# Optimization experiments

Hardware: AMD Instinct MI355X
Metric: run time of the kernel (lower is better)

## Reference

```python
import jax, jax.numpy as jnp
import numpy as np

B, L, D_MODEL = 2, 2048, 1024
EXPAND, D_STATE, D_CONV = 2, 16, 4
D_INNER = EXPAND * D_MODEL
DT_RANK = D_MODEL // 16  # mamba default: ceil(d_model/16)


def setup_inputs() -> dict:
    key = jax.random.key(0)
    ks = jax.random.split(key, 8)
    s = 0.02
    return {
        "x": jax.random.normal(ks[0], (B, L, D_MODEL), jnp.float32),
        "in_proj_w": jax.random.normal(ks[1], (2 * D_INNER, D_MODEL), jnp.float32) * s,
        "conv_w": jax.random.normal(ks[2], (D_INNER, D_CONV), jnp.float32) * s,
        "conv_b": jnp.zeros((D_INNER,), jnp.float32),
        "x_proj_w": jax.random.normal(ks[3], (DT_RANK + 2 * D_STATE, D_INNER), jnp.float32) * s,
        "dt_proj_w": jax.random.normal(ks[4], (D_INNER, DT_RANK), jnp.float32) * s,
        "dt_proj_b": jnp.full((D_INNER,), -4.6, jnp.float32),  # softplus(-4.6) ~ 0.01 dt init
        "A_log": jnp.log(jnp.broadcast_to(jnp.arange(1, D_STATE + 1, dtype=jnp.float32), (D_INNER, D_STATE))),
        "D": jnp.ones((D_INNER,), jnp.float32),
        "ssm_out_w": jax.random.normal(ks[5], (D_MODEL, D_INNER), jnp.float32) * s,
        "final_w": jax.random.normal(ks[6], (D_MODEL, D_MODEL), jnp.float32) * s,
        "final_b": jnp.zeros((D_MODEL,), jnp.float32),
    }


def _forward(x, in_proj_w, conv_w, conv_b, x_proj_w, dt_proj_w, dt_proj_b,
             A_log, D, ssm_out_w, final_w, final_b):
    d_inner, d_state = A_log.shape
    dt_rank = dt_proj_w.shape[1]
    d_conv = conv_w.shape[1]

    # in_proj -> split into x-branch and gate z  (B, L, 2*d_inner)
    xz = jnp.einsum('bld,ed->ble', x, in_proj_w)
    xin, z = jnp.split(xz, 2, axis=-1)

    # causal depthwise conv1d over time, then SiLU
    xc = jax.lax.conv_general_dilated(
        xin.swapaxes(1, 2),               # (B, d_inner, L)
        conv_w[:, None, :],               # (O=d_inner, I/g=1, W=d_conv)
        window_strides=(1,),
        padding=[(d_conv - 1, 0)],
        dimension_numbers=('NCH', 'OIH', 'NCH'),
        feature_group_count=d_inner,
    )
    xc = jax.nn.silu(xc + conv_b[None, :, None]).swapaxes(1, 2)  # (B, L, d_inner)

    # input-dependent SSM parameters
    x_dbl = jnp.einsum('bld,ed->ble', xc, x_proj_w)              # (B, L, dt_rank+2*d_state)
    dt, Bm, Cm = jnp.split(x_dbl, [dt_rank, dt_rank + d_state], axis=-1)
    delta = jax.nn.softplus(jnp.einsum('blr,dr->bld', dt, dt_proj_w) + dt_proj_b)  # (B,L,d_inner)
    A = -jnp.exp(A_log)                                          # (d_inner, d_state)

    # selective scan: h_t = exp(dt*A) h_{t-1} + dt*B_t*u_t ; y_t = <h_t, C_t>
    def step(h, t):
        delta_t, B_t, C_t, u_t = t                               # (B,Di), (B,N), (B,N), (B,Di)
        h = jnp.exp(delta_t[..., None] * A) * h + (delta_t * u_t)[..., None] * B_t[:, None, :]
        return h, jnp.einsum('bdn,bn->bd', h, C_t)

    h0 = jnp.zeros((x.shape[0], d_inner, d_state), x.dtype)
    xs = (delta.swapaxes(0, 1), Bm.swapaxes(0, 1), Cm.swapaxes(0, 1), xc.swapaxes(0, 1))
    _, ys = jax.lax.scan(step, h0, xs)                           # (L, B, d_inner)

    y = ys.swapaxes(0, 1) + xc * D                               # skip term D*u
    y = y * jax.nn.silu(z)                                       # gating
    out = jnp.einsum('bld,md->blm', y, ssm_out_w)                # Mamba out_proj -> d_model
    # wrapper: Linear(d_model, d_model) then SiLU
    return jax.nn.silu(jnp.einsum('blm,nm->bln', out, final_w) + final_b)


def reference(x, in_proj_w, conv_w, conv_b, x_proj_w, dt_proj_w, dt_proj_b,
              A_log, D, ssm_out_w, final_w, final_b):
    return _forward(x, in_proj_w, conv_w, conv_b, x_proj_w, dt_proj_w, dt_proj_b,
                    A_log, D, ssm_out_w, final_w, final_b)
```

## Files before the change

kernel.cpp:

```cpp
#include <hip/hip_runtime.h>
#include <hip/hip_bf16.h>
#include <math.h>

#define BB 2
#define LL 2048
#define DMODEL 1024
#define DINNER 2048
#define DSTATE 16
#define DCONV 4
#define DTRANK 64
#define MROWS (BB * LL)
#define XPROJ_N (DTRANK + 2 * DSTATE)

#define SEG 64
#define LS (LL / SEG)

#define XKSPLIT 8
#define XKC (DINNER / XKSPLIT)

typedef unsigned short ushort_t;
typedef short s8v __attribute__((ext_vector_type(8)));
typedef float f4v __attribute__((ext_vector_type(4)));

__device__ __forceinline__ float siluf(float x) {
    return x / (1.f + expf(-x));
}
__device__ __forceinline__ float softplusf(float x) {
    return fmaxf(x, 0.f) + log1pf(expf(-fabsf(x)));
}
__device__ __forceinline__ ushort_t f32_to_bf16(float f) {
    unsigned u = __builtin_bit_cast(unsigned, f);
    unsigned r = (u + 0x7FFFu + ((u >> 16) & 1u)) >> 16;
    return (ushort_t)r;
}
__device__ __forceinline__ float bf16_to_f32(ushort_t u) {
    return __builtin_bit_cast(float, ((unsigned)u) << 16);
}

__global__ __launch_bounds__(256) void prep_kernel(
    const float* __restrict__ x, const float* __restrict__ ipw,
    const float* __restrict__ sow, const float* __restrict__ fw,
    const float* __restrict__ xpw, const float* __restrict__ dtw,
    ushort_t* __restrict__ x_bf, ushort_t* __restrict__ ipw_bf,
    ushort_t* __restrict__ sow_bf, ushort_t* __restrict__ fw_bf,
    ushort_t* __restrict__ xpw_bf, ushort_t* __restrict__ dtw_bf,
    float4* __restrict__ xdbl_zero)
{
    const long i = ((long)blockIdx.x * 256 + threadIdx.x) * 4;
    const float* src; ushort_t* dst; long off;
    if      (i < 4194304L)  { src = x;   dst = x_bf;   off = i; }
    else if (i < 8388608L)  { src = ipw; dst = ipw_bf; off = i - 4194304L; }
    else if (i < 10485760L) { src = sow; dst = sow_bf; off = i - 8388608L; }
    else if (i < 11534336L) { src = fw;  dst = fw_bf;  off = i - 10485760L; }
    else if (i < 11730944L) { src = xpw; dst = xpw_bf; off = i - 11534336L; }
    else if (i < 11862016L) { src = dtw; dst = dtw_bf; off = i - 11730944L; }
    else { xdbl_zero[(i - 11862016L) >> 2] = make_float4(0.f, 0.f, 0.f, 0.f); return; }
    const float4 v = *reinterpret_cast<const float4*>(src + off);
    ushort_t o[4] = {f32_to_bf16(v.x), f32_to_bf16(v.y),
                     f32_to_bf16(v.z), f32_to_bf16(v.w)};
    *reinterpret_cast<uint2*>(dst + off) = *reinterpret_cast<uint2*>(o);
}

__global__ __launch_bounds__(256) void cast_dt_kernel(
    const float* __restrict__ xdbl, ushort_t* __restrict__ dtbf)
{
    const int i4 = (blockIdx.x * 256 + threadIdx.x) * 4;
    const int row = i4 >> 6;
    const int col = i4 & 63;
    const float4 v = *reinterpret_cast<const float4*>(&xdbl[(size_t)row * XPROJ_N + col]);
    ushort_t o[4] = {f32_to_bf16(v.x), f32_to_bf16(v.y),
                     f32_to_bf16(v.z), f32_to_bf16(v.w)};
    *reinterpret_cast<uint2*>(dtbf + i4) = *reinterpret_cast<uint2*>(o);
}

#define TM 128
#define TN 128
#define TBK 32

__global__ __launch_bounds__(512) void gemm_bf16_mfma(
    const ushort_t* __restrict__ A, int lda,
    const ushort_t* __restrict__ B, int ldb,
    int K,
    void* __restrict__ C0v, void* __restrict__ C1v, int splitN, int ldc,
    const float* __restrict__ bias, int act, int store_bf16)
{
    __shared__ __align__(16) ushort_t As[TM * TBK];
    __shared__ __align__(16) ushort_t Bs[TN * TBK];

    const int tid  = threadIdx.x;
    const int lane = tid & 63;
    const int w    = tid >> 6;
    const int wm   = w & 1;
    const int wn   = w >> 1;
    const int m0   = blockIdx.y * TM;
    const int n0   = blockIdx.x * TN;

    const int srow = lane >> 2;
    const int scol = (lane & 3) * 8;

    f4v acc[4][2] = {};

    for (int k0 = 0; k0 < K; k0 += TBK) {
        {
            const ushort_t* ga = A + (size_t)(m0 + w * 16 + srow) * lda + k0 + scol;
            __builtin_amdgcn_global_load_lds(
                (const __attribute__((address_space(1))) unsigned int*)ga,
                (__attribute__((address_space(3))) unsigned int*)(As + w * 512),
                16, 0, 0);
        }
        {
            const ushort_t* gb = B + (size_t)(n0 + w * 16 + srow) * ldb + k0 + scol;
            __builtin_amdgcn_global_load_lds(
                (const __attribute__((address_space(1))) unsigned int*)gb,
                (__attribute__((address_space(3))) unsigned int*)(Bs + w * 512),
                16, 0, 0);
        }
        __syncthreads();

        const int fr = lane & 15;
        const int kg = lane >> 4;
        s8v a[4], b[2];
        #pragma unroll
        for (int t = 0; t < 4; ++t)
            a[t] = *reinterpret_cast<const s8v*>(As + (wm * 64 + t * 16 + fr) * TBK + kg * 8);
        #pragma unroll
        for (int t = 0; t < 2; ++t)
            b[t] = *reinterpret_cast<const s8v*>(Bs + (wn * 32 + t * 16 + fr) * TBK + kg * 8);
        #pragma unroll
        for (int i = 0; i < 4; ++i)
            #pragma unroll
            for (int j = 0; j < 2; ++j)
                acc[i][j] = __builtin_amdgcn_mfma_f32_16x16x32_bf16(
                    a[i], b[j], acc[i][j], 0, 0, 0);
        __syncthreads();
    }

    const int rbase = (lane >> 4) * 4;
    const int cbase = lane & 15;
    #pragma unroll
    for (int i = 0; i < 4; ++i) {
        #pragma unroll
        for (int j = 0; j < 2; ++j) {
            const int row = m0 + wm * 64 + i * 16 + rbase;
            const int col = n0 + wn * 32 + j * 16 + cbase;
            void* Cp = C0v;
            int c2 = col;
            if (C1v && col >= splitN) { Cp = C1v; c2 = col - splitN; }
            const float bv = bias ? bias[col] : 0.f;
            #pragma unroll
            for (int r = 0; r < 4; ++r) {
                float v = acc[i][j][r] + bv;
                if (act == 1) v = siluf(v);
                else if (act == 2) v = softplusf(v);
                if (store_bf16)
                    ((ushort_t*)Cp)[(size_t)(row + r) * ldc + c2] = f32_to_bf16(v);
                else
                    ((float*)Cp)[(size_t)(row + r) * ldc + c2] = v;
            }
        }
    }
}

#define UM 64
#define UN 128

__global__ __launch_bounds__(512) void gemm64_bf16_mfma(
    const ushort_t* __restrict__ A, int lda,
    const ushort_t* __restrict__ B, int ldb,
    int K,
    void* __restrict__ C0v, int ldc,
    const float* __restrict__ bias, int act, int store_bf16)
{
    __shared__ __align__(16) ushort_t As[UM * TBK];
    __shared__ __align__(16) ushort_t Bs[UN * TBK];

    const int tid  = threadIdx.x;
    const int lane = tid & 63;
    const int w    = tid >> 6;
    const int wm   = w & 1;
    const int wn   = w >> 1;
    const int m0   = blockIdx.y * UM;
    const int n0   = blockIdx.x * UN;

    const int srow = lane >> 2;
    const int scol = (lane & 3) * 8;

    f4v acc[2][2] = {};

    for (int k0 = 0; k0 < K; k0 += TBK) {
        if (w < 4) {
            const ushort_t* ga = A + (size_t)(m0 + w * 16 + srow) * lda + k0 + scol;
            __builtin_amdgcn_global_load_lds(
                (const __attribute__((address_space(1))) unsigned int*)ga,
                (__attribute__((address_space(3))) unsigned int*)(As + w * 512),
                16, 0, 0);
        }
        {
            const ushort_t* gb = B + (size_t)(n0 + w * 16 + srow) * ldb + k0 + scol;
            __builtin_amdgcn_global_load_lds(
                (const __attribute__((address_space(1))) unsigned int*)gb,
                (__attribute__((address_space(3))) unsigned int*)(Bs + w * 512),
                16, 0, 0);
        }
        __syncthreads();

        const int fr = lane & 15;
        const int kg = lane >> 4;
        s8v a[2], b[2];
        #pragma unroll
        for (int t = 0; t < 2; ++t)
            a[t] = *reinterpret_cast<const s8v*>(As + (wm * 32 + t * 16 + fr) * TBK + kg * 8);
        #pragma unroll
        for (int t = 0; t < 2; ++t)
            b[t] = *reinterpret_cast<const s8v*>(Bs + (wn * 32 + t * 16 + fr) * TBK + kg * 8);
        #pragma unroll
        for (int i = 0; i < 2; ++i)
            #pragma unroll
            for (int j = 0; j < 2; ++j)
                acc[i][j] = __builtin_amdgcn_mfma_f32_16x16x32_bf16(
                    a[i], b[j], acc[i][j], 0, 0, 0);
        __syncthreads();
    }

    const int rbase = (lane >> 4) * 4;
    const int cbase = lane & 15;
    #pragma unroll
    for (int i = 0; i < 2; ++i) {
        #pragma unroll
        for (int j = 0; j < 2; ++j) {
            const int row = m0 + wm * 32 + i * 16 + rbase;
            const int col = n0 + wn * 32 + j * 16 + cbase;
            const float bv = bias ? bias[col] : 0.f;
            #pragma unroll
            for (int r = 0; r < 4; ++r) {
                float v = acc[i][j][r] + bv;
                if (act == 1) v = siluf(v);
                else if (act == 2) v = softplusf(v);
                if (store_bf16)
                    ((ushort_t*)C0v)[(size_t)(row + r) * ldc + col] = f32_to_bf16(v);
                else
                    ((float*)C0v)[(size_t)(row + r) * ldc + col] = v;
            }
        }
    }
}

__global__ __launch_bounds__(256) void xproj_mfma(
    const ushort_t* __restrict__ A, const ushort_t* __restrict__ Bw,
    float* __restrict__ Cout)
{
    __shared__ __align__(16) ushort_t As[64 * 32];
    __shared__ __align__(16) ushort_t Bs[96 * 32];

    const int tid = threadIdx.x;
    const int lane = tid & 63;
    const int w = tid >> 6;
    const int kbase = blockIdx.x * XKC;
    const int m0 = blockIdx.y * 64;

    const int srow = lane >> 2;
    const int scol = (lane & 3) * 8;

    f4v acc[6] = {};

    for (int k0 = kbase; k0 < kbase + XKC; k0 += 32) {
        {
            const ushort_t* ga = A + (size_t)(m0 + w * 16 + srow) * DINNER + k0 + scol;
            __builtin_amdgcn_global_load_lds(
                (const __attribute__((address_space(1))) unsigned int*)ga,
                (__attribute__((address_space(3))) unsigned int*)(As + (w * 16) * 32),
                16, 0, 0);
        }
        {
            const ushort_t* gb = Bw + (size_t)(w * 16 + srow) * DINNER + k0 + scol;
            __builtin_amdgcn_global_load_lds(
                (const __attribute__((address_space(1))) unsigned int*)gb,
                (__attribute__((address_space(3))) unsigned int*)(Bs + (w * 16) * 32),
                16, 0, 0);
        }
        if (w < 2) {
            const ushort_t* gb = Bw + (size_t)((4 + w) * 16 + srow) * DINNER + k0 + scol;
            __builtin_amdgcn_global_load_lds(
                (const __attribute__((address_space(1))) unsigned int*)gb,
                (__attribute__((address_space(3))) unsigned int*)(Bs + ((4 + w) * 16) * 32),
                16, 0, 0);
        }
        __syncthreads();

        const int fr = lane & 15;
        const int kg = lane >> 4;
        const s8v a = *reinterpret_cast<const s8v*>(As + (w * 16 + fr) * 32 + kg * 8);
        #pragma unroll
        for (int j = 0; j < 6; ++j) {
            const s8v b = *reinterpret_cast<const s8v*>(Bs + (j * 16 + fr) * 32 + kg * 8);
            acc[j] = __builtin_amdgcn_mfma_f32_16x16x32_bf16(a, b, acc[j], 0, 0, 0);
        }
        __syncthreads();
    }

    const int rbase = (lane >> 4) * 4;
    const int cb = lane & 15;
    #pragma unroll
    for (int j = 0; j < 6; ++j)
        #pragma unroll
        for (int r = 0; r < 4; ++r)
            atomicAdd(&Cout[(size_t)(m0 + w * 16 + rbase + r) * XPROJ_N + j * 16 + cb],
                      acc[j][r]);
}

__global__ __launch_bounds__(256) void conv_silu_kernel(
    const ushort_t* __restrict__ xin, const float* __restrict__ w,
    const float* __restrict__ b, ushort_t* __restrict__ xcbf)
{
    const int idx = blockIdx.x * blockDim.x + threadIdx.x;
    const int c = idx % DINNER;
    const int bl = idx / DINNER;
    const int l = bl % LL;
    const int bb = bl / LL;
    if (bb >= BB) return;

    const ushort_t* xp = xin + (size_t)bb * LL * DINNER + c;
    float acc = b[c];
    #pragma unroll
    for (int k = 0; k < DCONV; ++k) {
        const int ll = l - (DCONV - 1) + k;
        if (ll >= 0)
            acc = fmaf(bf16_to_f32(xp[(size_t)ll * DINNER]), w[c * DCONV + k], acc);
    }
    xcbf[idx] = f32_to_bf16(siluf(acc));
}

__global__ __launch_bounds__(256) void scan_part1(
    const ushort_t* __restrict__ delta, const float* __restrict__ xdbl,
    const ushort_t* __restrict__ xc, const float* __restrict__ A_log,
    float* __restrict__ hloc, float* __restrict__ decay)
{
    const int d = blockIdx.x * 256 + threadIdx.x;
    const int seg = blockIdx.y;
    const int b = blockIdx.z;
    const int t0 = seg * LS;

    float Ad[DSTATE];
    #pragma unroll
    for (int n = 0; n < DSTATE; ++n)
        Ad[n] = -expf(A_log[d * DSTATE + n]);

    float h[DSTATE];
    #pragma unroll
    for (int n = 0; n < DSTATE; ++n) h[n] = 0.f;

    const ushort_t* dp = delta + ((size_t)b * LL) * DINNER + d;
    const ushort_t* up = xc    + ((size_t)b * LL) * DINNER + d;
    const float*    xb = xdbl  + ((size_t)b * LL) * XPROJ_N;

    float sum_dl = 0.f;
    for (int t = t0; t < t0 + LS; ++t) {
        const float dl = bf16_to_f32(dp[(size_t)t * DINNER]);
        const float u  = bf16_to_f32(up[(size_t)t * DINNER]);
        const float4 b0 = *reinterpret_cast<const float4*>(&xb[t * XPROJ_N + DTRANK + 0]);
        const float4 b1 = *reinterpret_cast<const float4*>(&xb[t * XPROJ_N + DTRANK + 4]);
        const float4 b2 = *reinterpret_cast<const float4*>(&xb[t * XPROJ_N + DTRANK + 8]);
        const float4 b3 = *reinterpret_cast<const float4*>(&xb[t * XPROJ_N + DTRANK + 12]);
        const float Bv[DSTATE] = {b0.x, b0.y, b0.z, b0.w, b1.x, b1.y, b1.z, b1.w,
                                  b2.x, b2.y, b2.z, b2.w, b3.x, b3.y, b3.z, b3.w};
        const float dlu = dl * u;
        sum_dl += dl;
        #pragma unroll
        for (int n = 0; n < DSTATE; ++n)
            h[n] = __expf(dl * Ad[n]) * h[n] + dlu * Bv[n];
    }

    const size_t base = (((size_t)b * SEG + seg) * DSTATE) * DINNER + d;
    #pragma unroll
    for (int n = 0; n < DSTATE; ++n) {
        hloc[base + (size_t)n * DINNER]  = h[n];
        decay[base + (size_t)n * DINNER] = __expf(Ad[n] * sum_dl);
    }
}

__global__ __launch_bounds__(256) void scan_combine(
    float* __restrict__ hloc, const float* __restrict__ decay)
{
    const int idx = blockIdx.x * 256 + threadIdx.x;
    const int d = idx % DINNER;
    const int n = (idx / DINNER) % DSTATE;
    const int b = idx / (DINNER * DSTATE);
    if (b >= BB) return;

    float carry = 0.f;
    for (int s = 0; s < SEG; ++s) {
        const size_t off = (((size_t)b * SEG + s) * DSTATE + n) * DINNER + d;
        const float hl = hloc[off];
        hloc[off] = carry;
        carry = decay[off] * carry + hl;
    }
}

__global__ __launch_bounds__(256) void scan_part2(
    const ushort_t* __restrict__ delta, const float* __restrict__ xdbl,
    const ushort_t* __restrict__ xc, const ushort_t* __restrict__ z,
    const float* __restrict__ A_log, const float* __restrict__ Dvec,
    const float* __restrict__ hstart, ushort_t* __restrict__ ybf)
{
    const int d = blockIdx.x * 256 + threadIdx.x;
    const int seg = blockIdx.y;
    const int b = blockIdx.z;
    const int t0 = seg * LS;

    float Ad[DSTATE];
    #pragma unroll
    for (int n = 0; n < DSTATE; ++n)
        Ad[n] = -expf(A_log[d * DSTATE + n]);

    float h[DSTATE];
    const size_t hbase = (((size_t)b * SEG + seg) * DSTATE) * DINNER + d;
    #pragma unroll
    for (int n = 0; n < DSTATE; ++n)
        h[n] = hstart[hbase + (size_t)n * DINNER];

    const float Dd = Dvec[d];
    const ushort_t* dp = delta + ((size_t)b * LL) * DINNER + d;
    const ushort_t* up = xc    + ((size_t)b * LL) * DINNER + d;
    const float*    xb = xdbl  + ((size_t)b * LL) * XPROJ_N;
    const ushort_t* zp = z     + ((size_t)b * LL) * DINNER + d;
    ushort_t*       yp = ybf   + ((size_t)b * LL) * DINNER + d;

    for (int t = t0; t < t0 + LS; ++t) {
        const float dl = bf16_to_f32(dp[(size_t)t * DINNER]);
        const float u  = bf16_to_f32(up[(size_t)t * DINNER]);
        const float zv = bf16_to_f32(zp[(size_t)t * DINNER]);
        const float4 b0 = *reinterpret_cast<const float4*>(&xb[t * XPROJ_N + DTRANK + 0]);
        const float4 b1 = *reinterpret_cast<const float4*>(&xb[t * XPROJ_N + DTRANK + 4]);
        const float4 b2 = *reinterpret_cast<const float4*>(&xb[t * XPROJ_N + DTRANK + 8]);
        const float4 b3 = *reinterpret_cast<const float4*>(&xb[t * XPROJ_N + DTRANK + 12]);
        const float4 c0 = *reinterpret_cast<const float4*>(&xb[t * XPROJ_N + DTRANK + DSTATE + 0]);
        const float4 c1 = *reinterpret_cast<const float4*>(&xb[t * XPROJ_N + DTRANK + DSTATE + 4]);
        const float4 c2 = *reinterpret_cast<const float4*>(&xb[t * XPROJ_N + DTRANK + DSTATE + 8]);
        const float4 c3 = *reinterpret_cast<const float4*>(&xb[t * XPROJ_N + DTRANK + DSTATE + 12]);
        const float Bv[DSTATE] = {b0.x, b0.y, b0.z, b0.w, b1.x, b1.y, b1.z, b1.w,
                                  b2.x, b2.y, b2.z, b2.w, b3.x, b3.y, b3.z, b3.w};
        const float Cv[DSTATE] = {c0.x, c0.y, c0.z, c0.w, c1.x, c1.y, c1.z, c1.w,
                                  c2.x, c2.y, c2.z, c2.w, c3.x, c3.y, c3.z, c3.w};
        const float dlu = dl * u;
        float y = 0.f;
        #pragma unroll
        for (int n = 0; n < DSTATE; ++n) {
            h[n] = __expf(dl * Ad[n]) * h[n] + dlu * Bv[n];
            y = fmaf(h[n], Cv[n], y);
        }
        yp[(size_t)t * DINNER] = f32_to_bf16((y + u * Dd) * siluf(zv));
    }
}

extern "C" void kernel_launch(void* const* d_in, const int* in_sizes, int n_in,
                              void* d_out, int out_size, void* d_ws, size_t ws_size,
                              hipStream_t stream) {
    const float* x         = (const float*)d_in[0];
    const float* in_proj_w = (const float*)d_in[1];
    const float* conv_w    = (const float*)d_in[2];
    const float* conv_b    = (const float*)d_in[3];
    const float* x_proj_w  = (const float*)d_in[4];
    const float* dt_proj_w = (const float*)d_in[5];
    const float* dt_proj_b = (const float*)d_in[6];
    const float* A_log     = (const float*)d_in[7];
    const float* Dvec      = (const float*)d_in[8];
    const float* ssm_out_w = (const float*)d_in[9];
    const float* final_w   = (const float*)d_in[10];
    const float* final_b   = (const float*)d_in[11];
    float* out = (float*)d_out;

    const size_t MB = 1024 * 1024;
    char* base = (char*)d_ws;
    ushort_t* xin_bf   = (ushort_t*)(base);
    ushort_t* z_bf     = (ushort_t*)(base + 16 * MB);
    ushort_t* xc_bf    = (ushort_t*)(base + 32 * MB);
    ushort_t* delta_bf = (ushort_t*)(base + 48 * MB);
    float*    xdbl     = (float*)(base + 64 * MB);
    ushort_t* x_bf     = (ushort_t*)(base + 78 * MB);
    ushort_t* ipw_bf   = (ushort_t*)(base + 86 * MB);
    ushort_t* sow_bf   = (ushort_t*)(base + 94 * MB);
    ushort_t* fw_bf    = (ushort_t*)(base + 98 * MB);
    ushort_t* xpw_bf   = (ushort_t*)(base + 100 * MB);
    ushort_t* dtw_bf   = (ushort_t*)(base + 100 * MB + 512 * 1024);
    ushort_t* dt_bf    = (ushort_t*)(base + 101 * MB);
    ushort_t* y_bf     = (ushort_t*)(base + 102 * MB);
    ushort_t* outb_bf  = (ushort_t*)(base + 118 * MB);
    float* hloc  = (float*)(base);
    float* decay = (float*)(base + 78 * MB);

    prep_kernel<<<11968, 256, 0, stream>>>(
        x, in_proj_w, ssm_out_w, final_w, x_proj_w, dt_proj_w,
        x_bf, ipw_bf, sow_bf, fw_bf, xpw_bf, dtw_bf, (float4*)xdbl);

    gemm_bf16_mfma<<<dim3(2 * DINNER / TN, MROWS / TM), 512, 0, stream>>>(
        x_bf, DMODEL, ipw_bf, DMODEL, DMODEL,
        xin_bf, z_bf, DINNER, DINNER, nullptr, 0, 1);

    conv_silu_kernel<<<(MROWS * DINNER) / 256, 256, 0, stream>>>(
        xin_bf, conv_w, conv_b, xc_bf);

    xproj_mfma<<<dim3(XKSPLIT, MROWS / 64), 256, 0, stream>>>(xc_bf, xpw_bf, xdbl);

    cast_dt_kernel<<<(MROWS * DTRANK / 4) / 256, 256, 0, stream>>>(xdbl, dt_bf);
    gemm64_bf16_mfma<<<dim3(DINNER / UN, MROWS / UM), 512, 0, stream>>>(
        dt_bf, DTRANK, dtw_bf, DTRANK, DTRANK,
        delta_bf, DINNER, dt_proj_b, 2, 1);

    scan_part1<<<dim3(DINNER / 256, SEG, BB), 256, 0, stream>>>(
        delta_bf, xdbl, xc_bf, A_log, hloc, decay);
    scan_combine<<<(BB * DSTATE * DINNER) / 256, 256, 0, stream>>>(hloc, decay);
    scan_part2<<<dim3(DINNER / 256, SEG, BB), 256, 0, stream>>>(
        delta_bf, xdbl, xc_bf, z_bf, A_log, Dvec, hloc, y_bf);

    gemm64_bf16_mfma<<<dim3(DMODEL / UN, MROWS / UM), 512, 0, stream>>>(
        y_bf, DINNER, sow_bf, DINNER, DINNER,
        outb_bf, DMODEL, nullptr, 0, 1);

    gemm64_bf16_mfma<<<dim3(DMODEL / UN, MROWS / UM), 512, 0, stream>>>(
        outb_bf, DMODEL, fw_bf, DMODEL, DMODEL,
        out, DMODEL, final_b, 1, 0);
}
```

Baseline: 378.6 us.

## Replace in_proj GEMM with 256x256 multi-buffered swizzled MFMA kernel

```diff
diff --git a/kernel.cpp b/kernel.cpp
--- a/kernel.cpp
+++ b/kernel.cpp
@@ -73,83 +73,156 @@
     *reinterpret_cast<uint2*>(dtbf + i4) = *reinterpret_cast<uint2*>(o);
 }
 
-#define TM 128
-#define TN 128
 #define TBK 32
 
-__global__ __launch_bounds__(512) void gemm_bf16_mfma(
+__device__ __forceinline__ void stage_half(
+    const ushort_t* __restrict__ A, int lda,
+    const ushort_t* __restrict__ B, int ldb,
+    int m0, int n0, int g, char* sb, int tid, int w)
+{
+    const bool isA  = (g & 2) != 0;
+    const int  half = g & 1;
+    const int  tau  = g >> 2;
+    const int  slot = ((tau << 1) + half) & 3;
+    const int  r  = tid >> 2;
+    const int  kb = ((tid & 3) << 4) ^ (((tid >> 5) & 1) << 5);
+    const int  ke = kb >> 1;
+    const ushort_t* src = isA ? A : B;
+    const int  ld   = isA ? lda : ldb;
+    const int  row0 = (isA ? m0 : n0) + half * 128;
+    char* dst = sb + (isA ? 0 : 65536) + slot * 16384 + (w << 10);
+    const ushort_t* gp = src + (size_t)(row0 + r) * ld + tau * 64 + ke;
+    __builtin_amdgcn_global_load_lds(
+        (const __attribute__((address_space(1))) unsigned int*)gp,
+        (__attribute__((address_space(3))) unsigned int*)dst, 16, 0, 0);
+    __builtin_amdgcn_global_load_lds(
+        (const __attribute__((address_space(1))) unsigned int*)(gp + 32),
+        (__attribute__((address_space(3))) unsigned int*)(dst + 8192), 16, 0, 0);
+}
+
+#define MFMA_QUAD(MB, NB)                                                     \
+    _Pragma("unroll")                                                         \
+    for (int mi = 0; mi < 4; ++mi)                                            \
+      _Pragma("unroll")                                                       \
+      for (int nj = 0; nj < 2; ++nj)                                          \
+        _Pragma("unroll")                                                     \
+        for (int ks = 0; ks < 2; ++ks)                                        \
+          acc[(MB) + mi][(NB) + nj] = __builtin_amdgcn_mfma_f32_16x16x32_bf16(\
+              a[mi][ks], b[(NB) + nj][ks], acc[(MB) + mi][(NB) + nj], 0, 0, 0);
+
+__global__ void __launch_bounds__(512, 2) gemm256_bf16_mfma(
     const ushort_t* __restrict__ A, int lda,
     const ushort_t* __restrict__ B, int ldb,
     int K,
     void* __restrict__ C0v, void* __restrict__ C1v, int splitN, int ldc,
     const float* __restrict__ bias, int act, int store_bf16)
 {
-    __shared__ __align__(16) ushort_t As[TM * TBK];
-    __shared__ __align__(16) ushort_t Bs[TN * TBK];
+    __shared__ __align__(16) ushort_t smem[65536];
+    char* sb = (char*)smem;
 
     const int tid  = threadIdx.x;
     const int lane = tid & 63;
     const int w    = tid >> 6;
     const int wm   = w & 1;
     const int wn   = w >> 1;
-    const int m0   = blockIdx.y * TM;
-    const int n0   = blockIdx.x * TN;
-
-    const int srow = lane >> 2;
-    const int scol = (lane & 3) * 8;
-
-    f4v acc[4][2] = {};
-
-    for (int k0 = 0; k0 < K; k0 += TBK) {
-        {
-            const ushort_t* ga = A + (size_t)(m0 + w * 16 + srow) * lda + k0 + scol;
-            __builtin_amdgcn_global_load_lds(
-                (const __attribute__((address_space(1))) unsigned int*)ga,
-                (__attribute__((address_space(3))) unsigned int*)(As + w * 512),
-                16, 0, 0);
-        }
-        {
-            const ushort_t* gb = B + (size_t)(n0 + w * 16 + srow) * ldb + k0 + scol;
-            __builtin_amdgcn_global_load_lds(
-                (const __attribute__((address_space(1))) unsigned int*)gb,
-                (__attribute__((address_space(3))) unsigned int*)(Bs + w * 512),
-                16, 0, 0);
-        }
-        __syncthreads();
-
-        const int fr = lane & 15;
-        const int kg = lane >> 4;
-        s8v a[4], b[2];
-        #pragma unroll
-        for (int t = 0; t < 4; ++t)
-            a[t] = *reinterpret_cast<const s8v*>(As + (wm * 64 + t * 16 + fr) * TBK + kg * 8);
-        #pragma unroll
-        for (int t = 0; t < 2; ++t)
-            b[t] = *reinterpret_cast<const s8v*>(Bs + (wn * 32 + t * 16 + fr) * TBK + kg * 8);
-        #pragma unroll
-        for (int i = 0; i < 4; ++i)
+    const int m0   = blockIdx.y * 256;
+    const int n0   = blockIdx.x * 256;
+    const int fr   = lane & 15;
+    const int kg   = lane >> 4;
+    const int NT   = K >> 6;
+    const int glim = NT << 2;
+
+    const int laneoff = fr * 64 + ((kg * 16) ^ ((fr & 8) << 2));
+    const int halfB   = wn >> 1;
+
+    f4v acc[8][4] = {};
+    s8v a[4][2], b[4][2];
+
+    #pragma unroll
+    for (int g = 0; g < 7; ++g)
+        stage_half(A, lda, B, ldb, m0, n0, g, sb, tid, w);
+    asm volatile("s_waitcnt vmcnt(6)" ::: "memory");
+    __builtin_amdgcn_s_barrier();
+
+    for (int t = 0; t < NT; ++t) {
+        const int slotA = ((t << 1) + wm) & 3;
+        const int slotB = ((t << 1) + halfB) & 3;
+        const char* sa = sb + slotA * 16384;
+        const char* sB = sb + 65536 + slotB * 16384 + ((wn & 1) << 12);
+        const int gb = (t << 2) + 7;
+
+        #pragma unroll
+        for (int mi = 0; mi < 4; ++mi)
             #pragma unroll
-            for (int j = 0; j < 2; ++j)
-                acc[i][j] = __builtin_amdgcn_mfma_f32_16x16x32_bf16(
-                    a[i], b[j], acc[i][j], 0, 0, 0);
-        __syncthreads();
+            for (int ks = 0; ks < 2; ++ks)
+                a[mi][ks] = *reinterpret_cast<const s8v*>(
+                    sa + ks * 8192 + mi * 1024 + laneoff);
+        #pragma unroll
+        for (int nj = 0; nj < 4; ++nj)
+            #pragma unroll
+            for (int ks = 0; ks < 2; ++ks)
+                b[nj][ks] = *reinterpret_cast<const s8v*>(
+                    sB + ks * 8192 + nj * 1024 + laneoff);
+        if (gb < glim) stage_half(A, lda, B, ldb, m0, n0, gb, sb, tid, w);
+        __builtin_amdgcn_s_barrier();
+        asm volatile("s_waitcnt lgkmcnt(0)" ::: "memory");
+        __builtin_amdgcn_sched_barrier(0);
+        __builtin_amdgcn_s_setprio(1);
+        MFMA_QUAD(0, 0)
+        __builtin_amdgcn_s_setprio(0);
+        __builtin_amdgcn_s_barrier();
+
+        if (gb + 1 < glim) stage_half(A, lda, B, ldb, m0, n0, gb + 1, sb, tid, w);
+        __builtin_amdgcn_s_barrier();
+        __builtin_amdgcn_s_setprio(1);
+        MFMA_QUAD(0, 2)
+        __builtin_amdgcn_s_setprio(0);
+        __builtin_amdgcn_s_barrier();
+
+        #pragma unroll
+        for (int mi = 0; mi < 4; ++mi)
+            #pragma unroll
+            for (int ks = 0; ks < 2; ++ks)
+                a[mi][ks] = *reinterpret_cast<const s8v*>(
+                    sa + ks * 8192 + (mi + 4) * 1024 + laneoff);
+        if (gb + 2 < glim) stage_half(A, lda, B, ldb, m0, n0, gb + 2, sb, tid, w);
+        __builtin_amdgcn_s_barrier();
+        asm volatile("s_waitcnt lgkmcnt(0)" ::: "memory");
+        __builtin_amdgcn_sched_barrier(0);
+        __builtin_amdgcn_s_setprio(1);
+        MFMA_QUAD(4, 0)
+        __builtin_amdgcn_s_setprio(0);
+        __builtin_amdgcn_s_barrier();
+
+        if (gb + 3 < glim) stage_half(A, lda, B, ldb, m0, n0, gb + 3, sb, tid, w);
+        __builtin_amdgcn_s_barrier();
+        __builtin_amdgcn_s_setprio(1);
+        MFMA_QUAD(4, 2)
+        __builtin_amdgcn_s_setprio(0);
+        if (t < NT - 2) {
+            asm volatile("s_waitcnt vmcnt(6)" ::: "memory");
+            __builtin_amdgcn_s_barrier();
+        } else if (t == NT - 2) {
+            asm volatile("s_waitcnt vmcnt(0)" ::: "memory");
+            __builtin_amdgcn_s_barrier();
+        }
     }
 
     const int rbase = (lane >> 4) * 4;
     const int cbase = lane & 15;
     #pragma unroll
-    for (int i = 0; i < 4; ++i) {
-        #pragma unroll
-        for (int j = 0; j < 2; ++j) {
-            const int row = m0 + wm * 64 + i * 16 + rbase;
-            const int col = n0 + wn * 32 + j * 16 + cbase;
+    for (int mi = 0; mi < 8; ++mi) {
+        #pragma unroll
+        for (int nj = 0; nj < 4; ++nj) {
+            const int row = m0 + wm * 128 + mi * 16 + rbase;
+            const int col = n0 + wn * 64 + nj * 16 + cbase;
             void* Cp = C0v;
             int c2 = col;
             if (C1v && col >= splitN) { Cp = C1v; c2 = col - splitN; }
             const float bv = bias ? bias[col] : 0.f;
             #pragma unroll
             for (int r = 0; r < 4; ++r) {
-                float v = acc[i][j][r] + bv;
+                float v = acc[mi][nj][r] + bv;
                 if (act == 1) v = siluf(v);
                 else if (act == 2) v = softplusf(v);
                 if (store_bf16)
@@ -492,7 +565,7 @@
         x, in_proj_w, ssm_out_w, final_w, x_proj_w, dt_proj_w,
         x_bf, ipw_bf, sow_bf, fw_bf, xpw_bf, dtw_bf, (float4*)xdbl);
 
-    gemm_bf16_mfma<<<dim3(2 * DINNER / TN, MROWS / TM), 512, 0, stream>>>(
+    gemm256_bf16_mfma<<<dim3((2 * DINNER) / 256, MROWS / 256), 512, 0, stream>>>(
         x_bf, DMODEL, ipw_bf, DMODEL, DMODEL,
         xin_bf, z_bf, DINNER, DINNER, nullptr, 0, 1);
 
```

Measured after the change: 430.9 us. 13.8% more time.
